# Performance work log

Measured on AMD Instinct MI355X. Metric: run time of the kernel, lower is better.

The kernel has to match this reference:

```python
import jax, jax.numpy as jnp
import numpy as np

TAU_PRE = 2.0   # pre-synaptic trace time constant
SCALE = 1.0     # forward(scale=1.0) default
SPIKE_P = 0.1   # firing probability for realistic binary spike trains


def setup_inputs() -> dict:
    key = jax.random.key(0)
    k1, k2 = jax.random.split(key)
    T, B, NIN, NOUT = 2048, 128, 256, 128
    # binary spike trains, [T, B, N]
    in_spikes = (jax.random.uniform(k1, (T, B, NIN)) < SPIKE_P).astype(jnp.float32)
    out_spikes = (jax.random.uniform(k2, (T, B, NOUT)) < SPIKE_P).astype(jnp.float32)
    return {"in_spikes": in_spikes, "out_spikes": out_spikes}


def reference(in_spikes, out_spikes):
    # STDP.forward: loop over recorded timesteps, per step:
    #   trace_pre = trace_pre - trace_pre/tau_pre + in_spike          (decayed trace)
    #   dw = sum_b trace_pre[b, :] (outer) out_spike[b, :] -> [NOUT, NIN]
    #   delta_w += scale * dw
    # Expressed as a single lax.scan over the time axis.
    B, NIN = in_spikes.shape[1], in_spikes.shape[2]
    NOUT = out_spikes.shape[2]

    def step(carry, xs):
        trace_pre, delta_w = carry
        s_in, s_out = xs                                 # [B, NIN], [B, NOUT]
        trace_pre = trace_pre - trace_pre / TAU_PRE + s_in
        dw = jnp.einsum('bi,bo->oi', trace_pre, s_out)   # [NOUT, NIN]
        return (trace_pre, delta_w + SCALE * dw), None

    init = (jnp.zeros((B, NIN), in_spikes.dtype),
            jnp.zeros((NOUT, NIN), in_spikes.dtype))
    (_, delta_w), _ = jax.lax.scan(step, init, (in_spikes, out_spikes))
    return delta_w
```

## Files before the change

kernel.cpp:

```cpp
#include <hip/hip_runtime.h>
#include <hip/hip_bf16.h>

#define T_TOTAL 2048
#define BATCH   128
#define NIN     256
#define NOUT    128

#define TC      256
#define NTC     (T_TOTAL / TC)
#define BC      2
#define NBP     (BATCH / BC)
#define NBLOCKS (NBP * NTC)
#define WARM    32
#define CT      8
#define NCH     (TC / CT)

#define STRI    (BATCH * NIN)
#define STRO    (BATCH * NOUT)
#define OUT_ELEMS (NOUT * NIN)

typedef __attribute__((ext_vector_type(8)))  __bf16 bf16x8;
typedef __attribute__((ext_vector_type(2)))  __bf16 bf16x2;
typedef __attribute__((ext_vector_type(16))) float  f32x16;

static __device__ __forceinline__ unsigned pack_bf16(float a, float b) {
    bf16x2 v = { (__bf16)a, (__bf16)b };
    union { bf16x2 v; unsigned u; } c; c.v = v; return c.u;
}
static __device__ __forceinline__ bf16x8 frag4(unsigned w0, unsigned w1,
                                               unsigned w2, unsigned w3) {
    union { unsigned u[4]; bf16x8 f; } c;
    c.u[0] = w0; c.u[1] = w1; c.u[2] = w2; c.u[3] = w3; return c.f;
}

__global__ __launch_bounds__(512, 2)
void stdp_main(const float* __restrict__ in, const float* __restrict__ outs,
               float* __restrict__ dst, int use_atomic)
{
    const int tid  = threadIdx.x;
    const int lane = tid & 63;
    const int l31  = lane & 31;
    const int kh   = lane >> 5;
    const int nt   = tid >> 6;

    const int tc = blockIdx.x & 7;
    const int bp = blockIdx.x >> 3;
    const int b0 = bp * BC;
    const int t0 = tc * TC;

    const size_t in_off = (size_t)(b0 + kh) * NIN + nt * 32 + l31;
    const size_t ot_off = (size_t)(b0 + kh) * NOUT + l31;

    float tr = 0.f;

    if (tc > 0) {
        for (int t = t0 - WARM; t < t0; t += 8) {
            float v[8];
#pragma unroll
            for (int u = 0; u < 8; ++u) v[u] = in[(size_t)(t + u) * STRI + in_off];
#pragma unroll
            for (int u = 0; u < 8; ++u) tr = 0.5f * tr + v[u];
        }
    }

    f32x16 acc[4];
#pragma unroll
    for (int m = 0; m < 4; ++m) acc[m] = (f32x16)(0.f);

    float cin[8];
#pragma unroll
    for (int j = 0; j < 8; ++j) cin[j] = in[(size_t)(t0 + j) * STRI + in_off];

    for (int c = 0; c < NCH; ++c) {
        const int tb = t0 + c * CT;

        float af[4][8];
#pragma unroll
        for (int m = 0; m < 4; ++m)
#pragma unroll
            for (int j = 0; j < 8; ++j)
                af[m][j] = outs[(size_t)(tb + j) * STRO + ot_off + m * 32];

        float nin[8];
        if (c + 1 < NCH) {
#pragma unroll
            for (int j = 0; j < 8; ++j) nin[j] = in[(size_t)(tb + CT + j) * STRI + in_off];
        }

        unsigned bw[4];
#pragma unroll
        for (int p = 0; p < 4; ++p) {
            tr = 0.5f * tr + cin[2 * p];
            const float f0 = tr;
            tr = 0.5f * tr + cin[2 * p + 1];
            bw[p] = pack_bf16(f0, tr);
        }
        const bf16x8 bfrag = frag4(bw[0], bw[1], bw[2], bw[3]);

#pragma unroll
        for (int m = 0; m < 4; ++m) {
            const bf16x8 afrag = frag4(pack_bf16(af[m][0], af[m][1]),
                                       pack_bf16(af[m][2], af[m][3]),
                                       pack_bf16(af[m][4], af[m][5]),
                                       pack_bf16(af[m][6], af[m][7]));
            acc[m] = __builtin_amdgcn_mfma_f32_32x32x16_bf16(afrag, bfrag, acc[m], 0, 0, 0);
        }

#pragma unroll
        for (int j = 0; j < 8; ++j) cin[j] = nin[j];
    }

    if (use_atomic) {
#pragma unroll
        for (int m = 0; m < 4; ++m) {
            const int icol = nt * 32 + l31;
#pragma unroll
            for (int r = 0; r < 16; ++r) {
                const int row = (r & 3) + 8 * (r >> 2) + 4 * kh;
                atomicAdd(&dst[(m * 32 + row) * NIN + icol], acc[m][r]);
            }
        }
    } else {
        float* base = dst + (size_t)blockIdx.x * OUT_ELEMS;
#pragma unroll
        for (int m = 0; m < 4; ++m) {
            const int icol = nt * 32 + l31;
#pragma unroll
            for (int r = 0; r < 16; ++r) {
                const int row = (r & 3) + 8 * (r >> 2) + 4 * kh;
                base[(m * 32 + row) * NIN + icol] = acc[m][r];
            }
        }
    }
}

__global__ void zero_kernel(float* p, int n) {
    int i = blockIdx.x * blockDim.x + threadIdx.x;
    if (i < n) p[i] = 0.f;
}

__global__ __launch_bounds__(256)
void reduce_kernel(const float* __restrict__ ws, float* __restrict__ outp) {
    const int idx = blockIdx.x * 256 + threadIdx.x;
    float s = 0.f;
    for (int k = 0; k < NBLOCKS; k += 16) {
        float v[16];
#pragma unroll
        for (int u = 0; u < 16; ++u) v[u] = ws[(size_t)(k + u) * OUT_ELEMS + idx];
#pragma unroll
        for (int u = 0; u < 16; ++u) s += v[u];
    }
    outp[idx] = s;
}

extern "C" void kernel_launch(void* const* d_in, const int* in_sizes, int n_in,
                              void* d_out, int out_size, void* d_ws, size_t ws_size,
                              hipStream_t stream) {
    const float* in   = (const float*)d_in[0];
    const float* outs = (const float*)d_in[1];
    float* out = (float*)d_out;
    float* ws  = (float*)d_ws;

    if (ws_size >= (size_t)NBLOCKS * OUT_ELEMS * sizeof(float)) {
        stdp_main<<<NBLOCKS, 512, 0, stream>>>(in, outs, ws, 0);
        reduce_kernel<<<OUT_ELEMS / 256, 256, 0, stream>>>(ws, out);
    } else {
        zero_kernel<<<(OUT_ELEMS + 255) / 256, 256, 0, stream>>>(out, OUT_ELEMS);
        stdp_main<<<NBLOCKS, 512, 0, stream>>>(in, outs, out, 1);
    }
}
```

Before: 478.5 us.

## Split output rows across 16 waves, double-buffer loads, halve time chunks

Each block now runs 1024 threads, and the 128 output rows are split across two halves of waves, so each wave holds two MFMA accumulators instead of four. The time chunk doubles, which halves the block count and the partial-sum workspace the reduce kernel has to read. The outs and in loads for the next chunk are double-buffered in registers and prefetched one chunk ahead. In exchange, every trace value is recomputed by both wave halves, and the longer serial time chain per block reduces parallelism.

```diff
diff --git a/kernel.cpp b/kernel.cpp
--- a/kernel.cpp
+++ b/kernel.cpp
@@ -6,7 +6,7 @@
 #define NIN     256
 #define NOUT    128
 
-#define TC      256
+#define TC      512
 #define NTC     (T_TOTAL / TC)
 #define BC      2
 #define NBP     (BATCH / BC)
@@ -33,7 +33,7 @@
     c.u[0] = w0; c.u[1] = w1; c.u[2] = w2; c.u[3] = w3; return c.f;
 }
 
-__global__ __launch_bounds__(512, 2)
+__global__ __launch_bounds__(1024, 4)
 void stdp_main(const float* __restrict__ in, const float* __restrict__ outs,
                float* __restrict__ dst, int use_atomic)
 {
@@ -41,15 +41,17 @@
     const int lane = tid & 63;
     const int l31  = lane & 31;
     const int kh   = lane >> 5;
-    const int nt   = tid >> 6;
+    const int wv   = tid >> 6;
+    const int nt   = wv & 7;
+    const int mh   = wv >> 3;
 
-    const int tc = blockIdx.x & 7;
-    const int bp = blockIdx.x >> 3;
+    const int tc = blockIdx.x & 3;
+    const int bp = blockIdx.x >> 2;
     const int b0 = bp * BC;
     const int t0 = tc * TC;
 
     const size_t in_off = (size_t)(b0 + kh) * NIN + nt * 32 + l31;
-    const size_t ot_off = (size_t)(b0 + kh) * NOUT + l31;
+    const size_t ot_off = (size_t)(b0 + kh) * NOUT + mh * 64 + l31;
 
     float tr = 0.f;
 
@@ -63,74 +65,81 @@
         }
     }
 
-    f32x16 acc[4];
+    f32x16 acc[2];
+    acc[0] = (f32x16)(0.f);
+    acc[1] = (f32x16)(0.f);
+
+    float cin[2][8];
+    float af[2][2][8];
+
 #pragma unroll
-    for (int m = 0; m < 4; ++m) acc[m] = (f32x16)(0.f);
+    for (int j = 0; j < 8; ++j) cin[0][j] = in[(size_t)(t0 + j) * STRI + in_off];
+#pragma unroll
+    for (int mm = 0; mm < 2; ++mm)
+#pragma unroll
+        for (int j = 0; j < 8; ++j)
+            af[0][mm][j] = outs[(size_t)(t0 + j) * STRO + ot_off + mm * 32];
 
-    float cin[8];
-#pragma unroll
-    for (int j = 0; j < 8; ++j) cin[j] = in[(size_t)(t0 + j) * STRI + in_off];
+    auto body = [&](int cur, int c) {
+        const int tb  = t0 + c * CT;
+        const int nxt = cur ^ 1;
 
-    for (int c = 0; c < NCH; ++c) {
-        const int tb = t0 + c * CT;
-
-        float af[4][8];
-#pragma unroll
-        for (int m = 0; m < 4; ++m)
+        if (c + 1 < NCH) {
 #pragma unroll
             for (int j = 0; j < 8; ++j)
-                af[m][j] = outs[(size_t)(tb + j) * STRO + ot_off + m * 32];
-
-        float nin[8];
-        if (c + 1 < NCH) {
+                cin[nxt][j] = in[(size_t)(tb + CT + j) * STRI + in_off];
 #pragma unroll
-            for (int j = 0; j < 8; ++j) nin[j] = in[(size_t)(tb + CT + j) * STRI + in_off];
+            for (int mm = 0; mm < 2; ++mm)
+#pragma unroll
+                for (int j = 0; j < 8; ++j)
+                    af[nxt][mm][j] = outs[(size_t)(tb + CT + j) * STRO + ot_off + mm * 32];
         }
 
         unsigned bw[4];
 #pragma unroll
         for (int p = 0; p < 4; ++p) {
-            tr = 0.5f * tr + cin[2 * p];
+            tr = 0.5f * tr + cin[cur][2 * p];
             const float f0 = tr;
-            tr = 0.5f * tr + cin[2 * p + 1];
+            tr = 0.5f * tr + cin[cur][2 * p + 1];
             bw[p] = pack_bf16(f0, tr);
         }
         const bf16x8 bfrag = frag4(bw[0], bw[1], bw[2], bw[3]);
 
 #pragma unroll
-        for (int m = 0; m < 4; ++m) {
-            const bf16x8 afrag = frag4(pack_bf16(af[m][0], af[m][1]),
-                                       pack_bf16(af[m][2], af[m][3]),
-                                       pack_bf16(af[m][4], af[m][5]),
-                                       pack_bf16(af[m][6], af[m][7]));
-            acc[m] = __builtin_amdgcn_mfma_f32_32x32x16_bf16(afrag, bfrag, acc[m], 0, 0, 0);
+        for (int mm = 0; mm < 2; ++mm) {
+            const bf16x8 afrag = frag4(pack_bf16(af[cur][mm][0], af[cur][mm][1]),
+                                       pack_bf16(af[cur][mm][2], af[cur][mm][3]),
+                                       pack_bf16(af[cur][mm][4], af[cur][mm][5]),
+                                       pack_bf16(af[cur][mm][6], af[cur][mm][7]));
+            acc[mm] = __builtin_amdgcn_mfma_f32_32x32x16_bf16(afrag, bfrag, acc[mm], 0, 0, 0);
         }
+    };
 
-#pragma unroll
-        for (int j = 0; j < 8; ++j) cin[j] = nin[j];
+    for (int cc = 0; cc < NCH; cc += 2) {
+        body(0, cc);
+        body(1, cc + 1);
     }
 
+    const int icol = nt * 32 + l31;
     if (use_atomic) {
 #pragma unroll
-        for (int m = 0; m < 4; ++m) {
-            const int icol = nt * 32 + l31;
+        for (int mm = 0; mm < 2; ++mm)
 #pragma unroll
             for (int r = 0; r < 16; ++r) {
                 const int row = (r & 3) + 8 * (r >> 2) + 4 * kh;
-                atomicAdd(&dst[(m * 32 + row) * NIN + icol], acc[m][r]);
+                const int o   = mh * 64 + mm * 32 + row;
+                atomicAdd(&dst[o * NIN + icol], acc[mm][r]);
             }
-        }
     } else {
         float* base = dst + (size_t)blockIdx.x * OUT_ELEMS;
 #pragma unroll
-        for (int m = 0; m < 4; ++m) {
-            const int icol = nt * 32 + l31;
+        for (int mm = 0; mm < 2; ++mm)
 #pragma unroll
             for (int r = 0; r < 16; ++r) {
                 const int row = (r & 3) + 8 * (r >> 2) + 4 * kh;
-                base[(m * 32 + row) * NIN + icol] = acc[m][r];
+                const int o   = mh * 64 + mm * 32 + row;
+                base[o * NIN + icol] = acc[mm][r];
             }
-        }
     }
 }
 
@@ -162,10 +171,10 @@
     float* ws  = (float*)d_ws;
 
     if (ws_size >= (size_t)NBLOCKS * OUT_ELEMS * sizeof(float)) {
-        stdp_main<<<NBLOCKS, 512, 0, stream>>>(in, outs, ws, 0);
+        stdp_main<<<NBLOCKS, 1024, 0, stream>>>(in, outs, ws, 0);
         reduce_kernel<<<OUT_ELEMS / 256, 256, 0, stream>>>(ws, out);
     } else {
         zero_kernel<<<(OUT_ELEMS + 255) / 256, 256, 0, stream>>>(out, OUT_ELEMS);
-        stdp_main<<<NBLOCKS, 512, 0, stream>>>(in, outs, out, 1);
+        stdp_main<<<NBLOCKS, 1024, 0, stream>>>(in, outs, out, 1);
     }
 }
```

Result: no change. 477.5 us (-0.2%).
